# Performance work log

Measured on AMD Instinct MI355X. Metric: run time of the kernel, lower is better.

## Reference

```python
import jax, jax.numpy as jnp
import numpy as np

INPUT_DIM = 64
HIDDEN_DIM = 512
DIM_INNER = int(HIDDEN_DIM * 1.5)  # 768


def log_g(x):
    # torch.where(x >= 0, (relu(x) + 0.5).log(), -softplus(-x))
    return jnp.where(x >= 0, jnp.log(jax.nn.relu(x) + 0.5), -jax.nn.softplus(-x))


def setup_inputs() -> dict:
    key = jax.random.key(0)
    k_x, k1, k2, k3, k4 = jax.random.split(key, 5)
    B, S = 16, 4096
    x = jax.random.normal(k_x, (B, S, INPUT_DIM), dtype=jnp.float32)
    # weights stored as [in, out] (transpose of torch Linear.weight); bias=False everywhere
    W_in = jax.random.normal(k1, (INPUT_DIM, HIDDEN_DIM), dtype=jnp.float32) * 0.02
    W_hg = jax.random.normal(k2, (HIDDEN_DIM, 2 * DIM_INNER), dtype=jnp.float32) * 0.02
    W_out = jax.random.normal(k3, (DIM_INNER, HIDDEN_DIM), dtype=jnp.float32) * 0.02
    W_final = jax.random.normal(k4, (HIDDEN_DIM, 1), dtype=jnp.float32) * 0.02
    return {"x": x, "W_in": W_in, "W_hg": W_hg, "W_out": W_out, "W_final": W_final}


def reference(x, W_in, W_hg, W_out, W_final):
    # x: [B, S, input_dim]
    h = jnp.einsum('bsi,ih->bsh', x, W_in)                 # [B,S,H]
    hg = jnp.einsum('bsh,hd->bsd', h, W_hg)                # [B,S,2*DI]
    hidden, gate = jnp.split(hg, 2, axis=-1)               # each [B,S,DI]
    # seq_len > 1 path, prev_hidden=None
    log_coeffs = -jax.nn.softplus(gate)                    # log(1 - z)
    log_z = -jax.nn.softplus(-gate)                        # log(z)
    log_values = log_z + log_g(hidden)
    # heinsen associative scan in log space
    a_star = jnp.cumsum(log_coeffs, axis=1)
    log_h = a_star + jax.lax.cumlogsumexp(log_values - a_star, axis=1)
    out = jnp.exp(log_h)                                   # [B,S,DI]
    out = jnp.einsum('bsd,dh->bsh', out, W_out)            # [B,S,H]
    predictions = jnp.einsum('bsh,ho->bso', out, W_final)[..., 0]  # [B,S]
    return predictions
```

## Files before the change

kernel.cpp:

```cpp
#include <hip/hip_runtime.h>
#include <hip/hip_fp16.h>

typedef unsigned short u16;
typedef unsigned int   u32;
typedef __bf16 bf16x8 __attribute__((ext_vector_type(8)));
typedef float  f32x4  __attribute__((ext_vector_type(4)));

constexpr int BB   = 16;
constexpr int S    = 4096;
constexpr int M    = BB * S;
constexpr int DIN  = 64;
constexpr int H    = 512;
constexpr int DI   = 768;
constexpr int N2   = 1536;
constexpr int CL   = 128;
constexpr int NCHUNK = M / CL;
constexpr int SEGB  = S / 32;
constexpr int DTILES = 12;

constexpr size_t OFF_XB    = 0;
constexpr size_t OFF_B2C   = 8388608;
constexpr size_t OFF_WC    = 8585216;
constexpr size_t OFF_SEGC  = 8589312;
constexpr size_t OFF_SEGVH = 14880768;
constexpr size_t OFF_PART  = 21172224;

constexpr float L2E = 1.4426950408889634f;

__device__ __forceinline__ u16 f2bf(float f) {
  u32 u = __float_as_uint(f);
  u32 r = (u + 0x7FFFu + ((u >> 16) & 1u)) >> 16;
  return (u16)r;
}

__device__ __forceinline__ int cvs(int row, int d) {
  return row * 64 + (d ^ (((row >> 2) & 3) << 4));
}

__device__ __forceinline__ void act_cv(float hidden, float gate,
                                       float& cc, float& vv) {
  float eg  = __builtin_amdgcn_exp2f(gate * L2E);
  cc = __builtin_amdgcn_rcpf(1.0f + eg);
  float zz  = eg * cc;
  float gneg = __builtin_amdgcn_rcpf(
                  1.0f + __builtin_amdgcn_exp2f(-hidden * L2E));
  float gg  = (hidden >= 0.0f) ? (hidden + 0.5f) : gneg;
  vv = zz * gg;
}

__device__ __forceinline__ void comb_step(float& C, float& V, int bit, int ln) {
  float Cp = __shfl_xor(C, bit);
  float Vp = __shfl_xor(V, bit);
  bool up = (ln & bit) != 0;
  V = up ? fmaf(C, Vp, V) : fmaf(Cp, V, Vp);
  C *= Cp;
}

__global__ __launch_bounds__(256) void prep_xb(const float* __restrict__ x,
                                               u16* __restrict__ xb) {
  size_t i = (size_t)(blockIdx.x * 256 + threadIdx.x) * 8;
  float4 f0 = *(const float4*)(x + i);
  float4 f1 = *(const float4*)(x + i + 4);
  u32 w0 = f2bf(f0.x) | ((u32)f2bf(f0.y) << 16);
  u32 w1 = f2bf(f0.z) | ((u32)f2bf(f0.w) << 16);
  u32 w2 = f2bf(f1.x) | ((u32)f2bf(f1.y) << 16);
  u32 w3 = f2bf(f1.z) | ((u32)f2bf(f1.w) << 16);
  uint4 o = make_uint4(w0, w1, w2, w3);
  *(uint4*)(xb + i) = o;
}

__global__ __launch_bounds__(256) void prep_b2c(const float* __restrict__ Win,
                                                const float* __restrict__ Whg,
                                                u16* __restrict__ B2c) {
  __shared__ float Wl[64][65];
  const int tid = threadIdx.x;
  const int k = tid & 63;
  const int nloc = tid >> 6;
  const int n = blockIdx.x * 4 + nloc;
  const int g = n >> 5, r = n & 31;
  const int col = (r < 16) ? (g * 16 + r) : (DI + g * 16 + (r - 16));
  float acc = 0.f;
  for (int jc = 0; jc < H; jc += 64) {
    const int jl = tid & 63, k0 = tid >> 6;
    #pragma unroll
    for (int s = 0; s < 16; ++s) {
      int kr = k0 + 4 * s;
      Wl[kr][jl] = Win[kr * H + jc + jl];
    }
    __syncthreads();
    #pragma unroll 8
    for (int j = 0; j < 64; ++j)
      acc = fmaf(Wl[k][j], Whg[(size_t)(jc + j) * N2 + col], acc);
    __syncthreads();
  }
  B2c[n * 64 + k] = f2bf(acc);
}

__global__ __launch_bounds__(256) void prep_wcomb(const float* __restrict__ Wout,
                                                  const float* __restrict__ Wfin,
                                                  float* __restrict__ wc) {
  int wv = threadIdx.x >> 6, ln = threadIdx.x & 63;
  int d = blockIdx.x * 4 + wv;
  const float* row = Wout + (size_t)d * H;
  float s = 0.f;
  #pragma unroll
  for (int j = 0; j < 8; ++j) {
    int k = j * 64 + ln;
    s += row[k] * Wfin[k];
  }
  #pragma unroll
  for (int off = 32; off; off >>= 1) s += __shfl_xor(s, off);
  if (ln == 0) wc[d] = s;
}

template<int PASS>
__global__ __launch_bounds__(256) void fused_gemm_scan(
    const u16* __restrict__ xb, const u16* __restrict__ B2c,
    const float* __restrict__ Hin, const float* __restrict__ wcomb,
    float* __restrict__ SegC, float* __restrict__ SegV,
    float* __restrict__ part) {
  __shared__ __align__(16) u16 AB[16384];
  u32* cvl = (u32*)AB;

  const int tid = threadIdx.x, wv = tid >> 6, ln = tid & 63;
  const int nt = blockIdx.x % DTILES, ck = blockIdx.x / DTILES;
  const int m0 = ck * CL;
  const int wr = wv >> 1, wcol = wv & 1;
  const int lrow = ln & 15, hi4 = ln >> 4;

  {
    const uint4* gA = (const uint4*)(xb + (size_t)m0 * 64);
    const uint4* gB = (const uint4*)(B2c + (size_t)nt * 128 * 64);
    uint4* lA = (uint4*)AB;
    uint4* lB = (uint4*)(AB + 8192);
    #pragma unroll
    for (int j = 0; j < 4; ++j) {
      int q = j * 256 + tid;
      int qs = (q & ~7) | ((q & 7) ^ ((q >> 3) & 7));
      lA[qs] = gA[q];
      lB[qs] = gB[q];
    }
  }
  __syncthreads();

  f32x4 acc[4][4] = {};
  {
    const u16* Al = AB;
    const u16* Bl = AB + 8192;
    #pragma unroll
    for (int kk = 0; kk < 2; ++kk) {
      bf16x8 af[4], bfr[4];
      #pragma unroll
      for (int i = 0; i < 4; ++i) {
        int row = wr * 64 + i * 16 + lrow;
        af[i] = *(const bf16x8*)&Al[row * 64 + (((kk * 4 + hi4) ^ (row & 7)) << 3)];
      }
      #pragma unroll
      for (int j = 0; j < 4; ++j) {
        int row = wcol * 64 + j * 16 + lrow;
        bfr[j] = *(const bf16x8*)&Bl[row * 64 + (((kk * 4 + hi4) ^ (row & 7)) << 3)];
      }
      #pragma unroll
      for (int i = 0; i < 4; ++i)
        #pragma unroll
        for (int j = 0; j < 4; ++j)
          acc[i][j] = __builtin_amdgcn_mfma_f32_16x16x32_bf16(af[i], bfr[j], acc[i][j], 0, 0, 0);
    }
  }

  if (PASS == 1) {
    #pragma unroll
    for (int jp = 0; jp < 2; ++jp) {
      const int d = nt * 64 + (wcol * 2 + jp) * 16 + lrow;
      #pragma unroll
      for (int sl = 0; sl < 2; ++sl) {
        float Cr[2], Vr[2];
        #pragma unroll
        for (int ii = 0; ii < 2; ++ii) {
          const int i = sl * 2 + ii;
          float C = 1.f, V = 0.f;
          #pragma unroll
          for (int r = 0; r < 4; ++r) {
            float cc, vvv;
            act_cv(acc[i][2 * jp + 0][r], acc[i][2 * jp + 1][r], cc, vvv);
            V = fmaf(cc, V, vvv);
            C *= cc;
          }
          comb_step(C, V, 16, ln);
          comb_step(C, V, 32, ln);
          Cr[ii] = C; Vr[ii] = V;
        }
        float Cs = Cr[0] * Cr[1];
        float Vs = fmaf(Cr[1], Vr[0], Vr[1]);
        if (hi4 == 0) {
          int seg = ck * 4 + wr * 2 + sl;
          SegC[(size_t)seg * DI + d] = Cs;
          SegV[(size_t)seg * DI + d] = Vs;
        }
      }
    }
  } else {
    __syncthreads();

    #pragma unroll
    for (int i = 0; i < 4; ++i)
      #pragma unroll
      for (int jp = 0; jp < 2; ++jp) {
        const int dl = (wcol * 2 + jp) * 16 + lrow;
        #pragma unroll
        for (int r = 0; r < 4; ++r) {
          int row = wr * 64 + i * 16 + hi4 * 4 + r;
          float cc, vvv;
          act_cv(acc[i][2 * jp + 0][r], acc[i][2 * jp + 1][r], cc, vvv);
          __half2 p = __floats2half2_rn(cc, vvv);
          cvl[cvs(row, dl)] = *(const u32*)&p;
        }
      }
    __syncthreads();

    const int seg = ck * 4 + wv;
    float h = Hin[(size_t)seg * DI + nt * 64 + ln];
    const float wd = wcomb[nt * 64 + ln];
    #pragma unroll 4
    for (int tt = 0; tt < 32; ++tt) {
      const int t = wv * 32 + tt;
      u32 u = cvl[cvs(t, ln)];
      float hn;
      asm("v_fma_mix_f32 %0, %1, %2, %1 op_sel:[0,0,1] op_sel_hi:[1,0,1]"
          : "=v"(hn) : "v"(u), "v"(h));
      h = hn;
      float pv = h * wd;
      cvl[t * 64 + ((ln + t) & 63)] = __float_as_uint(pv);
    }
    __syncthreads();
    const int row = tid >> 1, half = tid & 1;
    float s = 0.f;
    #pragma unroll 8
    for (int jj = 0; jj < 32; ++jj) {
      int idx = (half * 32 + jj + row) & 63;
      s += __uint_as_float(cvl[row * 64 + idx]);
    }
    s += __shfl_xor(s, 1);
    if (half == 0) part[(size_t)nt * M + m0 + row] = s;
  }
}

__global__ __launch_bounds__(128) void scan_carry(const float* __restrict__ SegC,
                                                  float* __restrict__ SegVH) {
  const int b = blockIdx.x / 6, dc = blockIdx.x % 6;
  const int d = dc * 128 + threadIdx.x;
  const size_t base = (size_t)b * SEGB * DI + d;
  float carry = 0.f;
  for (int q0 = 0; q0 < SEGB; q0 += 16) {
    float c16[16], v16[16];
    #pragma unroll
    for (int j = 0; j < 16; ++j) {
      size_t idx = base + (size_t)(q0 + j) * DI;
      c16[j] = SegC[idx];
      v16[j] = SegVH[idx];
    }
    #pragma unroll
    for (int j = 0; j < 16; ++j) {
      size_t idx = base + (size_t)(q0 + j) * DI;
      SegVH[idx] = carry;
      carry = fmaf(c16[j], carry, v16[j]);
    }
  }
}

__global__ __launch_bounds__(256) void reduce12(const float* __restrict__ part,
                                                float* __restrict__ out) {
  int i = blockIdx.x * 256 + threadIdx.x;
  float s = 0.f;
  #pragma unroll
  for (int w = 0; w < DTILES; ++w) s += part[(size_t)w * M + i];
  out[i] = s;
}

extern "C" void kernel_launch(void* const* d_in, const int* in_sizes, int n_in,
                              void* d_out, int out_size, void* d_ws, size_t ws_size,
                              hipStream_t stream) {
  const float* x    = (const float*)d_in[0];
  const float* Win  = (const float*)d_in[1];
  const float* Whg  = (const float*)d_in[2];
  const float* Wout = (const float*)d_in[3];
  const float* Wfin = (const float*)d_in[4];
  float* out = (float*)d_out;
  char* ws = (char*)d_ws;

  u16*   xb    = (u16*)(ws + OFF_XB);
  u16*   B2c   = (u16*)(ws + OFF_B2C);
  float* wc    = (float*)(ws + OFF_WC);
  float* SegC  = (float*)(ws + OFF_SEGC);
  float* SegVH = (float*)(ws + OFF_SEGVH);
  float* part  = (float*)(ws + OFF_PART);

  prep_xb   <<<2048, 256, 0, stream>>>(x, xb);
  prep_b2c  <<<384,  256, 0, stream>>>(Win, Whg, B2c);
  prep_wcomb<<<192,  256, 0, stream>>>(Wout, Wfin, wc);
  fused_gemm_scan<1><<<NCHUNK * DTILES, 256, 0, stream>>>(xb, B2c, SegVH, wc, SegC, SegVH, part);
  scan_carry<<<96, 128, 0, stream>>>(SegC, SegVH);
  fused_gemm_scan<2><<<NCHUNK * DTILES, 256, 0, stream>>>(xb, B2c, SegVH, wc, SegC, SegVH, part);
  reduce12  <<<256,  256, 0, stream>>>(part, out);
}
```

Before: 137.4 us.

## Fuse two-pass GEMM scan into single pass with decoupled look-back carries

Replaces the two-pass approach (GEMM+segment summary, carry scan kernel, recomputed GEMM+scan) with one fused kernel. Blocks take ordered tickets, publish per-chunk carry summaries with a bitmask, and spin-wait for earlier chunks before running the local scan. The x to bf16 conversion is folded into the A-tile load, so the separate prep kernel goes away. This removes the duplicated GEMM and the extra launches, at the cost of serial dependency waits and global-memory spin polling. Each block rereads all prior carries (up to 31) rather than a running prefix.

Measured after the change: 382.2 us. +178.1%, slower.

```diff
diff --git a/kernel.cpp b/kernel.cpp
--- a/kernel.cpp
+++ b/kernel.cpp
@@ -9,21 +9,21 @@
 constexpr int BB   = 16;
 constexpr int S    = 4096;
 constexpr int M    = BB * S;
-constexpr int DIN  = 64;
 constexpr int H    = 512;
 constexpr int DI   = 768;
 constexpr int N2   = 1536;
 constexpr int CL   = 128;
-constexpr int NCHUNK = M / CL;
-constexpr int SEGB  = S / 32;
+constexpr int CKB  = S / CL;
 constexpr int DTILES = 12;
-
-constexpr size_t OFF_XB    = 0;
-constexpr size_t OFF_B2C   = 8388608;
-constexpr size_t OFF_WC    = 8585216;
-constexpr size_t OFF_SEGC  = 8589312;
-constexpr size_t OFF_SEGVH = 14880768;
-constexpr size_t OFF_PART  = 21172224;
+constexpr int NCHAIN = BB * DTILES;
+constexpr int NBLK = NCHAIN * CKB;
+
+constexpr size_t OFF_B2C    = 0;
+constexpr size_t OFF_WC     = 196608;
+constexpr size_t OFF_CTRL   = 200704;
+constexpr size_t OFF_CARRYC = 204800;
+constexpr size_t OFF_CARRYV = 1777664;
+constexpr size_t OFF_PART   = 3350528;
 
 constexpr float L2E = 1.4426950408889634f;
 
@@ -54,19 +54,6 @@
   bool up = (ln & bit) != 0;
   V = up ? fmaf(C, Vp, V) : fmaf(Cp, V, Vp);
   C *= Cp;
-}
-
-__global__ __launch_bounds__(256) void prep_xb(const float* __restrict__ x,
-                                               u16* __restrict__ xb) {
-  size_t i = (size_t)(blockIdx.x * 256 + threadIdx.x) * 8;
-  float4 f0 = *(const float4*)(x + i);
-  float4 f1 = *(const float4*)(x + i + 4);
-  u32 w0 = f2bf(f0.x) | ((u32)f2bf(f0.y) << 16);
-  u32 w1 = f2bf(f0.z) | ((u32)f2bf(f0.w) << 16);
-  u32 w2 = f2bf(f1.x) | ((u32)f2bf(f1.y) << 16);
-  u32 w3 = f2bf(f1.z) | ((u32)f2bf(f1.w) << 16);
-  uint4 o = make_uint4(w0, w1, w2, w3);
-  *(uint4*)(xb + i) = o;
 }
 
 __global__ __launch_bounds__(256) void prep_b2c(const float* __restrict__ Win,
@@ -113,31 +100,56 @@
   if (ln == 0) wc[d] = s;
 }
 
-template<int PASS>
-__global__ __launch_bounds__(256) void fused_gemm_scan(
-    const u16* __restrict__ xb, const u16* __restrict__ B2c,
-    const float* __restrict__ Hin, const float* __restrict__ wcomb,
-    float* __restrict__ SegC, float* __restrict__ SegV,
+__global__ __launch_bounds__(256) void fused_all(
+    const float* __restrict__ x, const u16* __restrict__ B2c,
+    const float* __restrict__ wcomb,
+    float* __restrict__ carryC, float* __restrict__ carryV,
+    u32* __restrict__ mask, u32* __restrict__ ticket,
     float* __restrict__ part) {
   __shared__ __align__(16) u16 AB[16384];
+  __shared__ float SCs[4][64], SVs[4][64];
+  __shared__ float hin_s[64];
+  __shared__ int tkt_s;
   u32* cvl = (u32*)AB;
 
   const int tid = threadIdx.x, wv = tid >> 6, ln = tid & 63;
-  const int nt = blockIdx.x % DTILES, ck = blockIdx.x / DTILES;
-  const int m0 = ck * CL;
+
+  if (tid == 0)
+    tkt_s = (int)__hip_atomic_fetch_add(ticket, 1u, __ATOMIC_RELAXED,
+                                        __HIP_MEMORY_SCOPE_AGENT);
+  __syncthreads();
+  const int logical = tkt_s;
+  const int c  = logical % NCHAIN;
+  const int ck = logical / NCHAIN;
+  const int b = c / DTILES, nt = c % DTILES;
+  const int m0 = b * S + ck * CL;
+
   const int wr = wv >> 1, wcol = wv & 1;
   const int lrow = ln & 15, hi4 = ln >> 4;
 
   {
-    const uint4* gA = (const uint4*)(xb + (size_t)m0 * 64);
+    const int row = tid >> 1, ch = (tid & 1) * 32;
+    const float4* gx = (const float4*)(x + (size_t)(m0 + row) * 64 + ch);
+    u32 w[16];
+    #pragma unroll
+    for (int j = 0; j < 8; ++j) {
+      float4 f = gx[j];
+      w[j * 2 + 0] = f2bf(f.x) | ((u32)f2bf(f.y) << 16);
+      w[j * 2 + 1] = f2bf(f.z) | ((u32)f2bf(f.w) << 16);
+    }
+    uint4* lA = (uint4*)AB;
+    #pragma unroll
+    for (int j2 = 0; j2 < 4; ++j2) {
+      int q = row * 8 + (tid & 1) * 4 + j2;
+      int qs = (q & ~7) | ((q & 7) ^ (row & 7));
+      lA[qs] = make_uint4(w[j2 * 4], w[j2 * 4 + 1], w[j2 * 4 + 2], w[j2 * 4 + 3]);
+    }
     const uint4* gB = (const uint4*)(B2c + (size_t)nt * 128 * 64);
-    uint4* lA = (uint4*)AB;
     uint4* lB = (uint4*)(AB + 8192);
     #pragma unroll
     for (int j = 0; j < 4; ++j) {
       int q = j * 256 + tid;
       int qs = (q & ~7) | ((q & 7) ^ ((q >> 3) & 7));
-      lA[qs] = gA[q];
       lB[qs] = gB[q];
     }
   }
@@ -168,104 +180,119 @@
     }
   }
 
-  if (PASS == 1) {
-    #pragma unroll
-    for (int jp = 0; jp < 2; ++jp) {
-      const int d = nt * 64 + (wcol * 2 + jp) * 16 + lrow;
-      #pragma unroll
-      for (int sl = 0; sl < 2; ++sl) {
-        float Cr[2], Vr[2];
-        #pragma unroll
-        for (int ii = 0; ii < 2; ++ii) {
-          const int i = sl * 2 + ii;
-          float C = 1.f, V = 0.f;
-          #pragma unroll
-          for (int r = 0; r < 4; ++r) {
-            float cc, vvv;
-            act_cv(acc[i][2 * jp + 0][r], acc[i][2 * jp + 1][r], cc, vvv);
-            V = fmaf(cc, V, vvv);
-            C *= cc;
-          }
-          comb_step(C, V, 16, ln);
-          comb_step(C, V, 32, ln);
-          Cr[ii] = C; Vr[ii] = V;
-        }
-        float Cs = Cr[0] * Cr[1];
-        float Vs = fmaf(Cr[1], Vr[0], Vr[1]);
-        if (hi4 == 0) {
-          int seg = ck * 4 + wr * 2 + sl;
-          SegC[(size_t)seg * DI + d] = Cs;
-          SegV[(size_t)seg * DI + d] = Vs;
-        }
-      }
-    }
-  } else {
-    __syncthreads();
-
-    #pragma unroll
-    for (int i = 0; i < 4; ++i)
-      #pragma unroll
-      for (int jp = 0; jp < 2; ++jp) {
-        const int dl = (wcol * 2 + jp) * 16 + lrow;
+  u32 cvp[4][2][4];
+  #pragma unroll
+  for (int jp = 0; jp < 2; ++jp) {
+    const int d = (wcol * 2 + jp) * 16 + lrow;
+    #pragma unroll
+    for (int sl = 0; sl < 2; ++sl) {
+      float Cr[2], Vr[2];
+      #pragma unroll
+      for (int ii = 0; ii < 2; ++ii) {
+        const int i = sl * 2 + ii;
+        float C = 1.f, V = 0.f;
         #pragma unroll
         for (int r = 0; r < 4; ++r) {
-          int row = wr * 64 + i * 16 + hi4 * 4 + r;
           float cc, vvv;
           act_cv(acc[i][2 * jp + 0][r], acc[i][2 * jp + 1][r], cc, vvv);
           __half2 p = __floats2half2_rn(cc, vvv);
-          cvl[cvs(row, dl)] = *(const u32*)&p;
+          cvp[i][jp][r] = *(const u32*)&p;
+          V = fmaf(cc, V, vvv);
+          C *= cc;
         }
-      }
-    __syncthreads();
-
-    const int seg = ck * 4 + wv;
-    float h = Hin[(size_t)seg * DI + nt * 64 + ln];
-    const float wd = wcomb[nt * 64 + ln];
-    #pragma unroll 4
-    for (int tt = 0; tt < 32; ++tt) {
-      const int t = wv * 32 + tt;
-      u32 u = cvl[cvs(t, ln)];
-      float hn;
-      asm("v_fma_mix_f32 %0, %1, %2, %1 op_sel:[0,0,1] op_sel_hi:[1,0,1]"
-          : "=v"(hn) : "v"(u), "v"(h));
-      h = hn;
-      float pv = h * wd;
-      cvl[t * 64 + ((ln + t) & 63)] = __float_as_uint(pv);
-    }
-    __syncthreads();
-    const int row = tid >> 1, half = tid & 1;
-    float s = 0.f;
-    #pragma unroll 8
-    for (int jj = 0; jj < 32; ++jj) {
-      int idx = (half * 32 + jj + row) & 63;
-      s += __uint_as_float(cvl[row * 64 + idx]);
-    }
-    s += __shfl_xor(s, 1);
-    if (half == 0) part[(size_t)nt * M + m0 + row] = s;
-  }
-}
-
-__global__ __launch_bounds__(128) void scan_carry(const float* __restrict__ SegC,
-                                                  float* __restrict__ SegVH) {
-  const int b = blockIdx.x / 6, dc = blockIdx.x % 6;
-  const int d = dc * 128 + threadIdx.x;
-  const size_t base = (size_t)b * SEGB * DI + d;
-  float carry = 0.f;
-  for (int q0 = 0; q0 < SEGB; q0 += 16) {
-    float c16[16], v16[16];
-    #pragma unroll
-    for (int j = 0; j < 16; ++j) {
-      size_t idx = base + (size_t)(q0 + j) * DI;
-      c16[j] = SegC[idx];
-      v16[j] = SegVH[idx];
-    }
-    #pragma unroll
-    for (int j = 0; j < 16; ++j) {
-      size_t idx = base + (size_t)(q0 + j) * DI;
-      SegVH[idx] = carry;
-      carry = fmaf(c16[j], carry, v16[j]);
-    }
-  }
+        comb_step(C, V, 16, ln);
+        comb_step(C, V, 32, ln);
+        Cr[ii] = C; Vr[ii] = V;
+      }
+      float Cs = Cr[0] * Cr[1];
+      float Vs = fmaf(Cr[1], Vr[0], Vr[1]);
+      if (hi4 == 0) {
+        int seg = wr * 2 + sl;
+        SCs[seg][d] = Cs;
+        SVs[seg][d] = Vs;
+      }
+    }
+  }
+  __syncthreads();
+
+  if (wv == 0) {
+    float C = SCs[0][ln], V = SVs[0][ln];
+    #pragma unroll
+    for (int s = 1; s < 4; ++s) {
+      V = fmaf(SCs[s][ln], V, SVs[s][ln]);
+      C *= SCs[s][ln];
+    }
+    if (ck < CKB - 1) {
+      carryC[(size_t)ck * (NCHAIN * 64) + c * 64 + ln] = C;
+      carryV[(size_t)ck * (NCHAIN * 64) + c * 64 + ln] = V;
+      __threadfence();
+      if (ln == 0)
+        __hip_atomic_fetch_or(&mask[c], 1u << ck, __ATOMIC_RELEASE,
+                              __HIP_MEMORY_SCOPE_AGENT);
+    }
+    float h = 0.f;
+    if (ck > 0) {
+      const u32 need = (1u << ck) - 1u;
+      while ((__hip_atomic_load(&mask[c], __ATOMIC_ACQUIRE,
+                                __HIP_MEMORY_SCOPE_AGENT) & need) != need)
+        __builtin_amdgcn_s_sleep(1);
+      const float* cC = carryC + c * 64 + ln;
+      const float* cV = carryV + c * 64 + ln;
+      for (int p0 = 0; p0 < ck; p0 += 8) {
+        float cb[8], vb[8];
+        #pragma unroll
+        for (int j = 0; j < 8; ++j)
+          if (p0 + j < ck) {
+            cb[j] = cC[(size_t)(p0 + j) * (NCHAIN * 64)];
+            vb[j] = cV[(size_t)(p0 + j) * (NCHAIN * 64)];
+          }
+        #pragma unroll
+        for (int j = 0; j < 8; ++j)
+          if (p0 + j < ck) h = fmaf(cb[j], h, vb[j]);
+      }
+    }
+    hin_s[ln] = h;
+  }
+
+  #pragma unroll
+  for (int i = 0; i < 4; ++i)
+    #pragma unroll
+    for (int jp = 0; jp < 2; ++jp) {
+      const int dl = (wcol * 2 + jp) * 16 + lrow;
+      #pragma unroll
+      for (int r = 0; r < 4; ++r) {
+        int row = wr * 64 + i * 16 + hi4 * 4 + r;
+        cvl[cvs(row, dl)] = cvp[i][jp][r];
+      }
+    }
+  __syncthreads();
+
+  float h = hin_s[ln];
+  if (wv >= 1) h = fmaf(SCs[0][ln], h, SVs[0][ln]);
+  if (wv >= 2) h = fmaf(SCs[1][ln], h, SVs[1][ln]);
+  if (wv >= 3) h = fmaf(SCs[2][ln], h, SVs[2][ln]);
+  const float wd = wcomb[nt * 64 + ln];
+  #pragma unroll 4
+  for (int tt = 0; tt < 32; ++tt) {
+    const int t = wv * 32 + tt;
+    u32 u = cvl[cvs(t, ln)];
+    float hn;
+    asm("v_fma_mix_f32 %0, %1, %2, %1 op_sel:[0,0,1] op_sel_hi:[1,0,1]"
+        : "=v"(hn) : "v"(u), "v"(h));
+    h = hn;
+    float pv = h * wd;
+    cvl[t * 64 + ((ln + t) & 63)] = __float_as_uint(pv);
+  }
+  __syncthreads();
+  const int row = tid >> 1, half = tid & 1;
+  float s = 0.f;
+  #pragma unroll 8
+  for (int jj = 0; jj < 32; ++jj) {
+    int idx = (half * 32 + jj + row) & 63;
+    s += __uint_as_float(cvl[row * 64 + idx]);
+  }
+  s += __shfl_xor(s, 1);
+  if (half == 0) part[(size_t)nt * M + m0 + row] = s;
 }
 
 __global__ __launch_bounds__(256) void reduce12(const float* __restrict__ part,
@@ -288,18 +315,17 @@
   float* out = (float*)d_out;
   char* ws = (char*)d_ws;
 
-  u16*   xb    = (u16*)(ws + OFF_XB);
-  u16*   B2c   = (u16*)(ws + OFF_B2C);
-  float* wc    = (float*)(ws + OFF_WC);
-  float* SegC  = (float*)(ws + OFF_SEGC);
-  float* SegVH = (float*)(ws + OFF_SEGVH);
-  float* part  = (float*)(ws + OFF_PART);
-
-  prep_xb   <<<2048, 256, 0, stream>>>(x, xb);
-  prep_b2c  <<<384,  256, 0, stream>>>(Win, Whg, B2c);
-  prep_wcomb<<<192,  256, 0, stream>>>(Wout, Wfin, wc);
-  fused_gemm_scan<1><<<NCHUNK * DTILES, 256, 0, stream>>>(xb, B2c, SegVH, wc, SegC, SegVH, part);
-  scan_carry<<<96, 128, 0, stream>>>(SegC, SegVH);
-  fused_gemm_scan<2><<<NCHUNK * DTILES, 256, 0, stream>>>(xb, B2c, SegVH, wc, SegC, SegVH, part);
-  reduce12  <<<256,  256, 0, stream>>>(part, out);
-}
+  u16*   B2c    = (u16*)(ws + OFF_B2C);
+  float* wc     = (float*)(ws + OFF_WC);
+  u32*   ticket = (u32*)(ws + OFF_CTRL);
+  u32*   mask   = (u32*)(ws + OFF_CTRL + 256);
+  float* carryC = (float*)(ws + OFF_CARRYC);
+  float* carryV = (float*)(ws + OFF_CARRYV);
+  float* part   = (float*)(ws + OFF_PART);
+
+  hipMemsetAsync(ws + OFF_CTRL, 0, 4096, stream);
+  prep_b2c  <<<384, 256, 0, stream>>>(Win, Whg, B2c);
+  prep_wcomb<<<192, 256, 0, stream>>>(Wout, Wfin, wc);
+  fused_all <<<NBLK, 256, 0, stream>>>(x, B2c, wc, carryC, carryV, mask, ticket, part);
+  reduce12  <<<256, 256, 0, stream>>>(part, out);
+}
```

## Fuse x conversion into pass one and optionally cache activation tiles globally

Applied to the files above, without the earlier changes.

The separate bf16 conversion kernel for x is removed. The first pass now reads fp32 x directly, converts it into shared memory, and, when the workspace is too small, also writes bf16 x for the second pass. When the workspace is large enough, pass one also stores the fp16 coefficient/value tiles to global memory, so pass two only reloads them and runs the scan instead of redoing the GEMM and activations. This trades recomputation for roughly 200 MB of extra global writes plus reads, and every column-tile block rereads and reconverts fp32 x.

Measured after the change: 145.8 us. +6.1%, slower.

```diff
diff --git a/kernel.cpp b/kernel.cpp
--- a/kernel.cpp
+++ b/kernel.cpp
@@ -9,7 +9,6 @@
 constexpr int BB   = 16;
 constexpr int S    = 4096;
 constexpr int M    = BB * S;
-constexpr int DIN  = 64;
 constexpr int H    = 512;
 constexpr int DI   = 768;
 constexpr int N2   = 1536;
@@ -17,13 +16,16 @@
 constexpr int NCHUNK = M / CL;
 constexpr int SEGB  = S / 32;
 constexpr int DTILES = 12;
-
-constexpr size_t OFF_XB    = 0;
-constexpr size_t OFF_B2C   = 8388608;
-constexpr size_t OFF_WC    = 8585216;
-constexpr size_t OFF_SEGC  = 8589312;
-constexpr size_t OFF_SEGVH = 14880768;
-constexpr size_t OFF_PART  = 21172224;
+constexpr int NBLK  = NCHUNK * DTILES;
+
+constexpr size_t OFF_B2C   = 0;
+constexpr size_t OFF_WC    = 196608;
+constexpr size_t OFF_SEGC  = 200704;
+constexpr size_t OFF_SEGVH = OFF_SEGC + 6291456;
+constexpr size_t OFF_PART  = OFF_SEGVH + 6291456;
+constexpr size_t OFF_AUX   = OFF_PART + 3145728;
+constexpr size_t CV_BYTES  = (size_t)NBLK * 32768;
+constexpr size_t NEED_CV   = OFF_AUX + CV_BYTES;
 
 constexpr float L2E = 1.4426950408889634f;
 
@@ -54,19 +56,6 @@
   bool up = (ln & bit) != 0;
   V = up ? fmaf(C, Vp, V) : fmaf(Cp, V, Vp);
   C *= Cp;
-}
-
-__global__ __launch_bounds__(256) void prep_xb(const float* __restrict__ x,
-                                               u16* __restrict__ xb) {
-  size_t i = (size_t)(blockIdx.x * 256 + threadIdx.x) * 8;
-  float4 f0 = *(const float4*)(x + i);
-  float4 f1 = *(const float4*)(x + i + 4);
-  u32 w0 = f2bf(f0.x) | ((u32)f2bf(f0.y) << 16);
-  u32 w1 = f2bf(f0.z) | ((u32)f2bf(f0.w) << 16);
-  u32 w2 = f2bf(f1.x) | ((u32)f2bf(f1.y) << 16);
-  u32 w3 = f2bf(f1.z) | ((u32)f2bf(f1.w) << 16);
-  uint4 o = make_uint4(w0, w1, w2, w3);
-  *(uint4*)(xb + i) = o;
 }
 
 __global__ __launch_bounds__(256) void prep_b2c(const float* __restrict__ Win,
@@ -113,12 +102,11 @@
   if (ln == 0) wc[d] = s;
 }
 
-template<int PASS>
-__global__ __launch_bounds__(256) void fused_gemm_scan(
-    const u16* __restrict__ xb, const u16* __restrict__ B2c,
-    const float* __restrict__ Hin, const float* __restrict__ wcomb,
+template<int MODE>
+__global__ __launch_bounds__(256) void fused_p1(
+    const float* __restrict__ x, const u16* __restrict__ B2c,
     float* __restrict__ SegC, float* __restrict__ SegV,
-    float* __restrict__ part) {
+    u32* __restrict__ cvg, u16* __restrict__ xb) {
   __shared__ __align__(16) u16 AB[16384];
   u32* cvl = (u32*)AB;
 
@@ -129,15 +117,34 @@
   const int lrow = ln & 15, hi4 = ln >> 4;
 
   {
-    const uint4* gA = (const uint4*)(xb + (size_t)m0 * 64);
+    const int row = tid >> 1, ch = (tid & 1) * 32;
+    const float4* gx = (const float4*)(x + (size_t)(m0 + row) * 64 + ch);
+    u32 w[16];
+    #pragma unroll
+    for (int j = 0; j < 8; ++j) {
+      float4 f = gx[j];
+      w[j * 2 + 0] = f2bf(f.x) | ((u32)f2bf(f.y) << 16);
+      w[j * 2 + 1] = f2bf(f.z) | ((u32)f2bf(f.w) << 16);
+    }
+    uint4* lA = (uint4*)AB;
+    #pragma unroll
+    for (int j2 = 0; j2 < 4; ++j2) {
+      int q = row * 8 + (tid & 1) * 4 + j2;
+      int qs = (q & ~7) | ((q & 7) ^ (row & 7));
+      lA[qs] = make_uint4(w[j2 * 4], w[j2 * 4 + 1], w[j2 * 4 + 2], w[j2 * 4 + 3]);
+    }
+    if (MODE == 0) {
+      uint4* gxb = (uint4*)(xb + (size_t)(m0 + row) * 64 + ch);
+      #pragma unroll
+      for (int j2 = 0; j2 < 4; ++j2)
+        gxb[j2] = make_uint4(w[j2 * 4], w[j2 * 4 + 1], w[j2 * 4 + 2], w[j2 * 4 + 3]);
+    }
     const uint4* gB = (const uint4*)(B2c + (size_t)nt * 128 * 64);
-    uint4* lA = (uint4*)AB;
     uint4* lB = (uint4*)(AB + 8192);
     #pragma unroll
     for (int j = 0; j < 4; ++j) {
       int q = j * 256 + tid;
       int qs = (q & ~7) | ((q & 7) ^ ((q >> 3) & 7));
-      lA[qs] = gA[q];
       lB[qs] = gB[q];
     }
   }
@@ -167,81 +174,51 @@
           acc[i][j] = __builtin_amdgcn_mfma_f32_16x16x32_bf16(af[i], bfr[j], acc[i][j], 0, 0, 0);
     }
   }
-
-  if (PASS == 1) {
-    #pragma unroll
-    for (int jp = 0; jp < 2; ++jp) {
-      const int d = nt * 64 + (wcol * 2 + jp) * 16 + lrow;
-      #pragma unroll
-      for (int sl = 0; sl < 2; ++sl) {
-        float Cr[2], Vr[2];
-        #pragma unroll
-        for (int ii = 0; ii < 2; ++ii) {
-          const int i = sl * 2 + ii;
-          float C = 1.f, V = 0.f;
-          #pragma unroll
-          for (int r = 0; r < 4; ++r) {
-            float cc, vvv;
-            act_cv(acc[i][2 * jp + 0][r], acc[i][2 * jp + 1][r], cc, vvv);
-            V = fmaf(cc, V, vvv);
-            C *= cc;
-          }
-          comb_step(C, V, 16, ln);
-          comb_step(C, V, 32, ln);
-          Cr[ii] = C; Vr[ii] = V;
-        }
-        float Cs = Cr[0] * Cr[1];
-        float Vs = fmaf(Cr[1], Vr[0], Vr[1]);
-        if (hi4 == 0) {
-          int seg = ck * 4 + wr * 2 + sl;
-          SegC[(size_t)seg * DI + d] = Cs;
-          SegV[(size_t)seg * DI + d] = Vs;
-        }
-      }
-    }
-  } else {
-    __syncthreads();
-
-    #pragma unroll
-    for (int i = 0; i < 4; ++i)
-      #pragma unroll
-      for (int jp = 0; jp < 2; ++jp) {
-        const int dl = (wcol * 2 + jp) * 16 + lrow;
+  __syncthreads();
+
+  #pragma unroll
+  for (int jp = 0; jp < 2; ++jp) {
+    const int dl = (wcol * 2 + jp) * 16 + lrow;
+    const int d = nt * 64 + dl;
+    #pragma unroll
+    for (int sl = 0; sl < 2; ++sl) {
+      float Cr[2], Vr[2];
+      #pragma unroll
+      for (int ii = 0; ii < 2; ++ii) {
+        const int i = sl * 2 + ii;
+        float C = 1.f, V = 0.f;
         #pragma unroll
         for (int r = 0; r < 4; ++r) {
-          int row = wr * 64 + i * 16 + hi4 * 4 + r;
           float cc, vvv;
           act_cv(acc[i][2 * jp + 0][r], acc[i][2 * jp + 1][r], cc, vvv);
-          __half2 p = __floats2half2_rn(cc, vvv);
-          cvl[cvs(row, dl)] = *(const u32*)&p;
+          if (MODE == 1) {
+            __half2 p = __floats2half2_rn(cc, vvv);
+            int row = wr * 64 + i * 16 + hi4 * 4 + r;
+            cvl[cvs(row, dl)] = *(const u32*)&p;
+          }
+          V = fmaf(cc, V, vvv);
+          C *= cc;
         }
-      }
+        comb_step(C, V, 16, ln);
+        comb_step(C, V, 32, ln);
+        Cr[ii] = C; Vr[ii] = V;
+      }
+      float Cs = Cr[0] * Cr[1];
+      float Vs = fmaf(Cr[1], Vr[0], Vr[1]);
+      if (hi4 == 0) {
+        int seg = ck * 4 + wr * 2 + sl;
+        SegC[(size_t)seg * DI + d] = Cs;
+        SegV[(size_t)seg * DI + d] = Vs;
+      }
+    }
+  }
+
+  if (MODE == 1) {
     __syncthreads();
-
-    const int seg = ck * 4 + wv;
-    float h = Hin[(size_t)seg * DI + nt * 64 + ln];
-    const float wd = wcomb[nt * 64 + ln];
-    #pragma unroll 4
-    for (int tt = 0; tt < 32; ++tt) {
-      const int t = wv * 32 + tt;
-      u32 u = cvl[cvs(t, ln)];
-      float hn;
-      asm("v_fma_mix_f32 %0, %1, %2, %1 op_sel:[0,0,1] op_sel_hi:[1,0,1]"
-          : "=v"(hn) : "v"(u), "v"(h));
-      h = hn;
-      float pv = h * wd;
-      cvl[t * 64 + ((ln + t) & 63)] = __float_as_uint(pv);
-    }
-    __syncthreads();
-    const int row = tid >> 1, half = tid & 1;
-    float s = 0.f;
-    #pragma unroll 8
-    for (int jj = 0; jj < 32; ++jj) {
-      int idx = (half * 32 + jj + row) & 63;
-      s += __uint_as_float(cvl[row * 64 + idx]);
-    }
-    s += __shfl_xor(s, 1);
-    if (half == 0) part[(size_t)nt * M + m0 + row] = s;
+    uint4* dst = (uint4*)(cvg + (size_t)blockIdx.x * 8192);
+    const uint4* src = (const uint4*)cvl;
+    #pragma unroll
+    for (int j = 0; j < 8; ++j) dst[j * 256 + tid] = src[j * 256 + tid];
   }
 }
 
@@ -266,6 +243,142 @@
       carry = fmaf(c16[j], carry, v16[j]);
     }
   }
+}
+
+__global__ __launch_bounds__(256) void fused_p2cv(
+    const u32* __restrict__ cvg, const float* __restrict__ Hin,
+    const float* __restrict__ wcomb, float* __restrict__ part) {
+  __shared__ __align__(16) u32 cvl[8192];
+  const int tid = threadIdx.x, wv = tid >> 6, ln = tid & 63;
+  const int nt = blockIdx.x % DTILES, ck = blockIdx.x / DTILES;
+  const int m0 = ck * CL;
+  {
+    const uint4* src = (const uint4*)(cvg + (size_t)blockIdx.x * 8192);
+    uint4* dst = (uint4*)cvl;
+    #pragma unroll
+    for (int j = 0; j < 8; ++j) dst[j * 256 + tid] = src[j * 256 + tid];
+  }
+  const int seg = ck * 4 + wv;
+  float h = Hin[(size_t)seg * DI + nt * 64 + ln];
+  const float wd = wcomb[nt * 64 + ln];
+  __syncthreads();
+  #pragma unroll 4
+  for (int tt = 0; tt < 32; ++tt) {
+    const int t = wv * 32 + tt;
+    u32 u = cvl[cvs(t, ln)];
+    float hn;
+    asm("v_fma_mix_f32 %0, %1, %2, %1 op_sel:[0,0,1] op_sel_hi:[1,0,1]"
+        : "=v"(hn) : "v"(u), "v"(h));
+    h = hn;
+    float pv = h * wd;
+    cvl[t * 64 + ((ln + t) & 63)] = __float_as_uint(pv);
+  }
+  __syncthreads();
+  const int row = tid >> 1, half = tid & 1;
+  float s = 0.f;
+  #pragma unroll 8
+  for (int jj = 0; jj < 32; ++jj) {
+    int idx = (half * 32 + jj + row) & 63;
+    s += __uint_as_float(cvl[row * 64 + idx]);
+  }
+  s += __shfl_xor(s, 1);
+  if (half == 0) part[(size_t)nt * M + m0 + row] = s;
+}
+
+__global__ __launch_bounds__(256) void fused_p2xb(
+    const u16* __restrict__ xb, const u16* __restrict__ B2c,
+    const float* __restrict__ Hin, const float* __restrict__ wcomb,
+    float* __restrict__ part) {
+  __shared__ __align__(16) u16 AB[16384];
+  u32* cvl = (u32*)AB;
+
+  const int tid = threadIdx.x, wv = tid >> 6, ln = tid & 63;
+  const int nt = blockIdx.x % DTILES, ck = blockIdx.x / DTILES;
+  const int m0 = ck * CL;
+  const int wr = wv >> 1, wcol = wv & 1;
+  const int lrow = ln & 15, hi4 = ln >> 4;
+
+  {
+    const uint4* gA = (const uint4*)(xb + (size_t)m0 * 64);
+    const uint4* gB = (const uint4*)(B2c + (size_t)nt * 128 * 64);
+    uint4* lA = (uint4*)AB;
+    uint4* lB = (uint4*)(AB + 8192);
+    #pragma unroll
+    for (int j = 0; j < 4; ++j) {
+      int q = j * 256 + tid;
+      int qs = (q & ~7) | ((q & 7) ^ ((q >> 3) & 7));
+      lA[qs] = gA[q];
+      lB[qs] = gB[q];
+    }
+  }
+  __syncthreads();
+
+  f32x4 acc[4][4] = {};
+  {
+    const u16* Al = AB;
+    const u16* Bl = AB + 8192;
+    #pragma unroll
+    for (int kk = 0; kk < 2; ++kk) {
+      bf16x8 af[4], bfr[4];
+      #pragma unroll
+      for (int i = 0; i < 4; ++i) {
+        int row = wr * 64 + i * 16 + lrow;
+        af[i] = *(const bf16x8*)&Al[row * 64 + (((kk * 4 + hi4) ^ (row & 7)) << 3)];
+      }
+      #pragma unroll
+      for (int j = 0; j < 4; ++j) {
+        int row = wcol * 64 + j * 16 + lrow;
+        bfr[j] = *(const bf16x8*)&Bl[row * 64 + (((kk * 4 + hi4) ^ (row & 7)) << 3)];
+      }
+      #pragma unroll
+      for (int i = 0; i < 4; ++i)
+        #pragma unroll
+        for (int j = 0; j < 4; ++j)
+          acc[i][j] = __builtin_amdgcn_mfma_f32_16x16x32_bf16(af[i], bfr[j], acc[i][j], 0, 0, 0);
+    }
+  }
+  __syncthreads();
+
+  #pragma unroll
+  for (int i = 0; i < 4; ++i)
+    #pragma unroll
+    for (int jp = 0; jp < 2; ++jp) {
+      const int dl = (wcol * 2 + jp) * 16 + lrow;
+      #pragma unroll
+      for (int r = 0; r < 4; ++r) {
+        int row = wr * 64 + i * 16 + hi4 * 4 + r;
+        float cc, vvv;
+        act_cv(acc[i][2 * jp + 0][r], acc[i][2 * jp + 1][r], cc, vvv);
+        __half2 p = __floats2half2_rn(cc, vvv);
+        cvl[cvs(row, dl)] = *(const u32*)&p;
+      }
+    }
+  __syncthreads();
+
+  const int seg = ck * 4 + wv;
+  float h = Hin[(size_t)seg * DI + nt * 64 + ln];
+  const float wd = wcomb[nt * 64 + ln];
+  #pragma unroll 4
+  for (int tt = 0; tt < 32; ++tt) {
+    const int t = wv * 32 + tt;
+    u32 u = cvl[cvs(t, ln)];
+    float hn;
+    asm("v_fma_mix_f32 %0, %1, %2, %1 op_sel:[0,0,1] op_sel_hi:[1,0,1]"
+        : "=v"(hn) : "v"(u), "v"(h));
+    h = hn;
+    float pv = h * wd;
+    cvl[t * 64 + ((ln + t) & 63)] = __float_as_uint(pv);
+  }
+  __syncthreads();
+  const int row = tid >> 1, half = tid & 1;
+  float s = 0.f;
+  #pragma unroll 8
+  for (int jj = 0; jj < 32; ++jj) {
+    int idx = (half * 32 + jj + row) & 63;
+    s += __uint_as_float(cvl[row * 64 + idx]);
+  }
+  s += __shfl_xor(s, 1);
+  if (half == 0) part[(size_t)nt * M + m0 + row] = s;
 }
 
 __global__ __launch_bounds__(256) void reduce12(const float* __restrict__ part,
@@ -288,18 +401,25 @@
   float* out = (float*)d_out;
   char* ws = (char*)d_ws;
 
-  u16*   xb    = (u16*)(ws + OFF_XB);
   u16*   B2c   = (u16*)(ws + OFF_B2C);
   float* wc    = (float*)(ws + OFF_WC);
   float* SegC  = (float*)(ws + OFF_SEGC);
   float* SegVH = (float*)(ws + OFF_SEGVH);
   float* part  = (float*)(ws + OFF_PART);
-
-  prep_xb   <<<2048, 256, 0, stream>>>(x, xb);
-  prep_b2c  <<<384,  256, 0, stream>>>(Win, Whg, B2c);
-  prep_wcomb<<<192,  256, 0, stream>>>(Wout, Wfin, wc);
-  fused_gemm_scan<1><<<NCHUNK * DTILES, 256, 0, stream>>>(xb, B2c, SegVH, wc, SegC, SegVH, part);
-  scan_carry<<<96, 128, 0, stream>>>(SegC, SegVH);
-  fused_gemm_scan<2><<<NCHUNK * DTILES, 256, 0, stream>>>(xb, B2c, SegVH, wc, SegC, SegVH, part);
-  reduce12  <<<256,  256, 0, stream>>>(part, out);
-}
+  const bool big = (ws_size >= NEED_CV);
+
+  prep_b2c  <<<384, 256, 0, stream>>>(Win, Whg, B2c);
+  prep_wcomb<<<192, 256, 0, stream>>>(Wout, Wfin, wc);
+  if (big) {
+    u32* cvg = (u32*)(ws + OFF_AUX);
+    fused_p1<1><<<NBLK, 256, 0, stream>>>(x, B2c, SegC, SegVH, cvg, nullptr);
+    scan_carry<<<96, 128, 0, stream>>>(SegC, SegVH);
+    fused_p2cv<<<NBLK, 256, 0, stream>>>(cvg, SegVH, wc, part);
+  } else {
+    u16* xb = (u16*)(ws + OFF_AUX);
+    fused_p1<0><<<NBLK, 256, 0, stream>>>(x, B2c, SegC, SegVH, nullptr, xb);
+    scan_carry<<<96, 128, 0, stream>>>(SegC, SegVH);
+    fused_p2xb<<<NBLK, 256, 0, stream>>>(xb, B2c, SegVH, wc, part);
+  }
+  reduce12<<<256, 256, 0, stream>>>(part, out);
+}
```

## Fuse bf16 conversion of x into GEMM kernels and simplify activation math

Applied to the files above, without the earlier changes.

Drops the separate prep_xb pass and converts fp32 x to bf16 while staging each tile in the fused kernels, using v_cvt_pk_bf16_f32. The activation is rewritten to share a single reciprocal between the gate and hidden sigmoids, and the fp16 packing now uses round-toward-zero cvt_pkrtz. In pass 2 the Hin and wcomb loads are issued before the GEMM so their latency overlaps it. In exchange, each of the 12 column-tile blocks per chunk now reads x in fp32 (twice the bytes of bf16), in both passes.

New measurement: 188.9 us. 37.4% more time.

```diff
diff --git a/kernel.cpp b/kernel.cpp
--- a/kernel.cpp
+++ b/kernel.cpp
@@ -9,7 +9,6 @@
 constexpr int BB   = 16;
 constexpr int S    = 4096;
 constexpr int M    = BB * S;
-constexpr int DIN  = 64;
 constexpr int H    = 512;
 constexpr int DI   = 768;
 constexpr int N2   = 1536;
@@ -17,20 +16,30 @@
 constexpr int NCHUNK = M / CL;
 constexpr int SEGB  = S / 32;
 constexpr int DTILES = 12;
-
-constexpr size_t OFF_XB    = 0;
-constexpr size_t OFF_B2C   = 8388608;
-constexpr size_t OFF_WC    = 8585216;
-constexpr size_t OFF_SEGC  = 8589312;
-constexpr size_t OFF_SEGVH = 14880768;
-constexpr size_t OFF_PART  = 21172224;
+constexpr int NBLK  = NCHUNK * DTILES;
+
+constexpr size_t OFF_B2C   = 0;
+constexpr size_t OFF_WC    = 196608;
+constexpr size_t OFF_SEGC  = 200704;
+constexpr size_t OFF_SEGVH = OFF_SEGC + 6291456;
+constexpr size_t OFF_PART  = OFF_SEGVH + 6291456;
 
 constexpr float L2E = 1.4426950408889634f;
 
 __device__ __forceinline__ u16 f2bf(float f) {
   u32 u = __float_as_uint(f);
-  u32 r = (u + 0x7FFFu + ((u >> 16) & 1u)) >> 16;
-  return (u16)r;
+  return (u16)((u + 0x7FFFu + ((u >> 16) & 1u)) >> 16);
+}
+
+__device__ __forceinline__ u32 pk_bf16(float lo, float hi) {
+  u32 r;
+  asm("v_cvt_pk_bf16_f32 %0, %1, %2" : "=v"(r) : "v"(lo), "v"(hi));
+  return r;
+}
+
+__device__ __forceinline__ u32 pk_f16(float lo, float hi) {
+  auto p = __builtin_amdgcn_cvt_pkrtz(lo, hi);
+  return *(const u32*)&p;
 }
 
 __device__ __forceinline__ int cvs(int row, int d) {
@@ -39,13 +48,13 @@
 
 __device__ __forceinline__ void act_cv(float hidden, float gate,
                                        float& cc, float& vv) {
-  float eg  = __builtin_amdgcn_exp2f(gate * L2E);
-  cc = __builtin_amdgcn_rcpf(1.0f + eg);
-  float zz  = eg * cc;
-  float gneg = __builtin_amdgcn_rcpf(
-                  1.0f + __builtin_amdgcn_exp2f(-hidden * L2E));
-  float gg  = (hidden >= 0.0f) ? (hidden + 0.5f) : gneg;
-  vv = zz * gg;
+  float eg = __builtin_amdgcn_exp2f(gate * L2E);
+  float eh = __builtin_amdgcn_exp2f(hidden * L2E);
+  float A = 1.0f + eg, B = 1.0f + eh;
+  float R = __builtin_amdgcn_rcpf(A * B);
+  cc = B * R;
+  float w = (hidden >= 0.0f) ? (hidden + 0.5f) * B : eh;
+  vv = eg * R * w;
 }
 
 __device__ __forceinline__ void comb_step(float& C, float& V, int bit, int ln) {
@@ -56,17 +65,63 @@
   C *= Cp;
 }
 
-__global__ __launch_bounds__(256) void prep_xb(const float* __restrict__ x,
-                                               u16* __restrict__ xb) {
-  size_t i = (size_t)(blockIdx.x * 256 + threadIdx.x) * 8;
-  float4 f0 = *(const float4*)(x + i);
-  float4 f1 = *(const float4*)(x + i + 4);
-  u32 w0 = f2bf(f0.x) | ((u32)f2bf(f0.y) << 16);
-  u32 w1 = f2bf(f0.z) | ((u32)f2bf(f0.w) << 16);
-  u32 w2 = f2bf(f1.x) | ((u32)f2bf(f1.y) << 16);
-  u32 w3 = f2bf(f1.z) | ((u32)f2bf(f1.w) << 16);
-  uint4 o = make_uint4(w0, w1, w2, w3);
-  *(uint4*)(xb + i) = o;
+__device__ __forceinline__ void stage_mfma(const float* __restrict__ x,
+                                           const u16* __restrict__ B2c,
+                                           u16* AB, int tid, int m0, int nt,
+                                           f32x4 (&acc)[4][4]) {
+  const int wv = tid >> 6, ln = tid & 63;
+  const int wr = wv >> 1, wcol = wv & 1;
+  const int lrow = ln & 15, hi4 = ln >> 4;
+  {
+    const int row = tid >> 1, ch = (tid & 1) * 32;
+    const float4* gx = (const float4*)(x + (size_t)(m0 + row) * 64 + ch);
+    u32 w[16];
+    #pragma unroll
+    for (int j = 0; j < 8; ++j) {
+      float4 f = gx[j];
+      w[j * 2 + 0] = pk_bf16(f.x, f.y);
+      w[j * 2 + 1] = pk_bf16(f.z, f.w);
+    }
+    uint4* lA = (uint4*)AB;
+    #pragma unroll
+    for (int j2 = 0; j2 < 4; ++j2) {
+      int q = row * 8 + (tid & 1) * 4 + j2;
+      int qs = (q & ~7) | ((q & 7) ^ (row & 7));
+      lA[qs] = make_uint4(w[j2 * 4], w[j2 * 4 + 1], w[j2 * 4 + 2], w[j2 * 4 + 3]);
+    }
+    const uint4* gB = (const uint4*)(B2c + (size_t)nt * 128 * 64);
+    uint4* lB = (uint4*)(AB + 8192);
+    #pragma unroll
+    for (int j = 0; j < 4; ++j) {
+      int q = j * 256 + tid;
+      int qs = (q & ~7) | ((q & 7) ^ ((q >> 3) & 7));
+      lB[qs] = gB[q];
+    }
+  }
+  __syncthreads();
+  {
+    const u16* Al = AB;
+    const u16* Bl = AB + 8192;
+    #pragma unroll
+    for (int kk = 0; kk < 2; ++kk) {
+      bf16x8 af[4], bfr[4];
+      #pragma unroll
+      for (int i = 0; i < 4; ++i) {
+        int row = wr * 64 + i * 16 + lrow;
+        af[i] = *(const bf16x8*)&Al[row * 64 + (((kk * 4 + hi4) ^ (row & 7)) << 3)];
+      }
+      #pragma unroll
+      for (int j = 0; j < 4; ++j) {
+        int row = wcol * 64 + j * 16 + lrow;
+        bfr[j] = *(const bf16x8*)&Bl[row * 64 + (((kk * 4 + hi4) ^ (row & 7)) << 3)];
+      }
+      #pragma unroll
+      for (int i = 0; i < 4; ++i)
+        #pragma unroll
+        for (int j = 0; j < 4; ++j)
+          acc[i][j] = __builtin_amdgcn_mfma_f32_16x16x32_bf16(af[i], bfr[j], acc[i][j], 0, 0, 0);
+    }
+  }
 }
 
 __global__ __launch_bounds__(256) void prep_b2c(const float* __restrict__ Win,
@@ -113,135 +168,48 @@
   if (ln == 0) wc[d] = s;
 }
 
-template<int PASS>
-__global__ __launch_bounds__(256) void fused_gemm_scan(
-    const u16* __restrict__ xb, const u16* __restrict__ B2c,
-    const float* __restrict__ Hin, const float* __restrict__ wcomb,
-    float* __restrict__ SegC, float* __restrict__ SegV,
-    float* __restrict__ part) {
+__global__ __launch_bounds__(256) void fused_p1(
+    const float* __restrict__ x, const u16* __restrict__ B2c,
+    float* __restrict__ SegC, float* __restrict__ SegV) {
   __shared__ __align__(16) u16 AB[16384];
-  u32* cvl = (u32*)AB;
-
   const int tid = threadIdx.x, wv = tid >> 6, ln = tid & 63;
   const int nt = blockIdx.x % DTILES, ck = blockIdx.x / DTILES;
   const int m0 = ck * CL;
   const int wr = wv >> 1, wcol = wv & 1;
   const int lrow = ln & 15, hi4 = ln >> 4;
 
-  {
-    const uint4* gA = (const uint4*)(xb + (size_t)m0 * 64);
-    const uint4* gB = (const uint4*)(B2c + (size_t)nt * 128 * 64);
-    uint4* lA = (uint4*)AB;
-    uint4* lB = (uint4*)(AB + 8192);
-    #pragma unroll
-    for (int j = 0; j < 4; ++j) {
-      int q = j * 256 + tid;
-      int qs = (q & ~7) | ((q & 7) ^ ((q >> 3) & 7));
-      lA[qs] = gA[q];
-      lB[qs] = gB[q];
-    }
-  }
-  __syncthreads();
-
   f32x4 acc[4][4] = {};
-  {
-    const u16* Al = AB;
-    const u16* Bl = AB + 8192;
-    #pragma unroll
-    for (int kk = 0; kk < 2; ++kk) {
-      bf16x8 af[4], bfr[4];
-      #pragma unroll
-      for (int i = 0; i < 4; ++i) {
-        int row = wr * 64 + i * 16 + lrow;
-        af[i] = *(const bf16x8*)&Al[row * 64 + (((kk * 4 + hi4) ^ (row & 7)) << 3)];
-      }
-      #pragma unroll
-      for (int j = 0; j < 4; ++j) {
-        int row = wcol * 64 + j * 16 + lrow;
-        bfr[j] = *(const bf16x8*)&Bl[row * 64 + (((kk * 4 + hi4) ^ (row & 7)) << 3)];
-      }
-      #pragma unroll
-      for (int i = 0; i < 4; ++i)
-        #pragma unroll
-        for (int j = 0; j < 4; ++j)
-          acc[i][j] = __builtin_amdgcn_mfma_f32_16x16x32_bf16(af[i], bfr[j], acc[i][j], 0, 0, 0);
-    }
-  }
-
-  if (PASS == 1) {
-    #pragma unroll
-    for (int jp = 0; jp < 2; ++jp) {
-      const int d = nt * 64 + (wcol * 2 + jp) * 16 + lrow;
-      #pragma unroll
-      for (int sl = 0; sl < 2; ++sl) {
-        float Cr[2], Vr[2];
-        #pragma unroll
-        for (int ii = 0; ii < 2; ++ii) {
-          const int i = sl * 2 + ii;
-          float C = 1.f, V = 0.f;
-          #pragma unroll
-          for (int r = 0; r < 4; ++r) {
-            float cc, vvv;
-            act_cv(acc[i][2 * jp + 0][r], acc[i][2 * jp + 1][r], cc, vvv);
-            V = fmaf(cc, V, vvv);
-            C *= cc;
-          }
-          comb_step(C, V, 16, ln);
-          comb_step(C, V, 32, ln);
-          Cr[ii] = C; Vr[ii] = V;
-        }
-        float Cs = Cr[0] * Cr[1];
-        float Vs = fmaf(Cr[1], Vr[0], Vr[1]);
-        if (hi4 == 0) {
-          int seg = ck * 4 + wr * 2 + sl;
-          SegC[(size_t)seg * DI + d] = Cs;
-          SegV[(size_t)seg * DI + d] = Vs;
-        }
-      }
-    }
-  } else {
-    __syncthreads();
-
-    #pragma unroll
-    for (int i = 0; i < 4; ++i)
-      #pragma unroll
-      for (int jp = 0; jp < 2; ++jp) {
-        const int dl = (wcol * 2 + jp) * 16 + lrow;
+  stage_mfma(x, B2c, AB, tid, m0, nt, acc);
+
+  #pragma unroll
+  for (int jp = 0; jp < 2; ++jp) {
+    const int d = nt * 64 + (wcol * 2 + jp) * 16 + lrow;
+    #pragma unroll
+    for (int sl = 0; sl < 2; ++sl) {
+      float Cr[2], Vr[2];
+      #pragma unroll
+      for (int ii = 0; ii < 2; ++ii) {
+        const int i = sl * 2 + ii;
+        float C = 1.f, V = 0.f;
         #pragma unroll
         for (int r = 0; r < 4; ++r) {
-          int row = wr * 64 + i * 16 + hi4 * 4 + r;
           float cc, vvv;
           act_cv(acc[i][2 * jp + 0][r], acc[i][2 * jp + 1][r], cc, vvv);
-          __half2 p = __floats2half2_rn(cc, vvv);
-          cvl[cvs(row, dl)] = *(const u32*)&p;
+          V = fmaf(cc, V, vvv);
+          C *= cc;
         }
-      }
-    __syncthreads();
-
-    const int seg = ck * 4 + wv;
-    float h = Hin[(size_t)seg * DI + nt * 64 + ln];
-    const float wd = wcomb[nt * 64 + ln];
-    #pragma unroll 4
-    for (int tt = 0; tt < 32; ++tt) {
-      const int t = wv * 32 + tt;
-      u32 u = cvl[cvs(t, ln)];
-      float hn;
-      asm("v_fma_mix_f32 %0, %1, %2, %1 op_sel:[0,0,1] op_sel_hi:[1,0,1]"
-          : "=v"(hn) : "v"(u), "v"(h));
-      h = hn;
-      float pv = h * wd;
-      cvl[t * 64 + ((ln + t) & 63)] = __float_as_uint(pv);
-    }
-    __syncthreads();
-    const int row = tid >> 1, half = tid & 1;
-    float s = 0.f;
-    #pragma unroll 8
-    for (int jj = 0; jj < 32; ++jj) {
-      int idx = (half * 32 + jj + row) & 63;
-      s += __uint_as_float(cvl[row * 64 + idx]);
-    }
-    s += __shfl_xor(s, 1);
-    if (half == 0) part[(size_t)nt * M + m0 + row] = s;
+        comb_step(C, V, 16, ln);
+        comb_step(C, V, 32, ln);
+        Cr[ii] = C; Vr[ii] = V;
+      }
+      float Cs = Cr[0] * Cr[1];
+      float Vs = fmaf(Cr[1], Vr[0], Vr[1]);
+      if (hi4 == 0) {
+        int seg = ck * 4 + wr * 2 + sl;
+        SegC[(size_t)seg * DI + d] = Cs;
+        SegV[(size_t)seg * DI + d] = Vs;
+      }
+    }
   }
 }
 
@@ -266,6 +234,64 @@
       carry = fmaf(c16[j], carry, v16[j]);
     }
   }
+}
+
+__global__ __launch_bounds__(256) void fused_p2(
+    const float* __restrict__ x, const u16* __restrict__ B2c,
+    const float* __restrict__ Hin, const float* __restrict__ wcomb,
+    float* __restrict__ part) {
+  __shared__ __align__(16) u16 AB[16384];
+  u32* cvl = (u32*)AB;
+  const int tid = threadIdx.x, wv = tid >> 6, ln = tid & 63;
+  const int nt = blockIdx.x % DTILES, ck = blockIdx.x / DTILES;
+  const int m0 = ck * CL;
+  const int wr = wv >> 1, wcol = wv & 1;
+  const int lrow = ln & 15, hi4 = ln >> 4;
+
+  const int seg = ck * 4 + wv;
+  float h = Hin[(size_t)seg * DI + nt * 64 + ln];
+  const float wd = wcomb[nt * 64 + ln];
+
+  f32x4 acc[4][4] = {};
+  stage_mfma(x, B2c, AB, tid, m0, nt, acc);
+  __syncthreads();
+
+  #pragma unroll
+  for (int i = 0; i < 4; ++i)
+    #pragma unroll
+    for (int jp = 0; jp < 2; ++jp) {
+      const int dl = (wcol * 2 + jp) * 16 + lrow;
+      #pragma unroll
+      for (int r = 0; r < 4; ++r) {
+        int row = wr * 64 + i * 16 + hi4 * 4 + r;
+        float cc, vvv;
+        act_cv(acc[i][2 * jp + 0][r], acc[i][2 * jp + 1][r], cc, vvv);
+        cvl[cvs(row, dl)] = pk_f16(cc, vvv);
+      }
+    }
+  __syncthreads();
+
+  #pragma unroll 4
+  for (int tt = 0; tt < 32; ++tt) {
+    const int t = wv * 32 + tt;
+    u32 u = cvl[cvs(t, ln)];
+    float hn;
+    asm("v_fma_mix_f32 %0, %1, %2, %1 op_sel:[0,0,1] op_sel_hi:[1,0,1]"
+        : "=v"(hn) : "v"(u), "v"(h));
+    h = hn;
+    float pv = h * wd;
+    cvl[t * 64 + ((ln + t) & 63)] = __float_as_uint(pv);
+  }
+  __syncthreads();
+  const int row = tid >> 1, half = tid & 1;
+  float s = 0.f;
+  #pragma unroll 8
+  for (int jj = 0; jj < 32; ++jj) {
+    int idx = (half * 32 + jj + row) & 63;
+    s += __uint_as_float(cvl[row * 64 + idx]);
+  }
+  s += __shfl_xor(s, 1);
+  if (half == 0) part[(size_t)nt * M + m0 + row] = s;
 }
 
 __global__ __launch_bounds__(256) void reduce12(const float* __restrict__ part,
@@ -288,18 +314,16 @@
   float* out = (float*)d_out;
   char* ws = (char*)d_ws;
 
-  u16*   xb    = (u16*)(ws + OFF_XB);
   u16*   B2c   = (u16*)(ws + OFF_B2C);
   float* wc    = (float*)(ws + OFF_WC);
   float* SegC  = (float*)(ws + OFF_SEGC);
   float* SegVH = (float*)(ws + OFF_SEGVH);
   float* part  = (float*)(ws + OFF_PART);
 
-  prep_xb   <<<2048, 256, 0, stream>>>(x, xb);
-  prep_b2c  <<<384,  256, 0, stream>>>(Win, Whg, B2c);
-  prep_wcomb<<<192,  256, 0, stream>>>(Wout, Wfin, wc);
-  fused_gemm_scan<1><<<NCHUNK * DTILES, 256, 0, stream>>>(xb, B2c, SegVH, wc, SegC, SegVH, part);
+  prep_b2c  <<<384, 256, 0, stream>>>(Win, Whg, B2c);
+  prep_wcomb<<<192, 256, 0, stream>>>(Wout, Wfin, wc);
+  fused_p1  <<<NBLK, 256, 0, stream>>>(x, B2c, SegC, SegVH);
   scan_carry<<<96, 128, 0, stream>>>(SegC, SegVH);
-  fused_gemm_scan<2><<<NCHUNK * DTILES, 256, 0, stream>>>(xb, B2c, SegVH, wc, SegC, SegVH, part);
-  reduce12  <<<256,  256, 0, stream>>>(part, out);
-}
+  fused_p2  <<<NBLK, 256, 0, stream>>>(x, B2c, SegVH, wc, part);
+  reduce12  <<<256, 256, 0, stream>>>(part, out);
+}
```
